# Performance work log

Hardware: AMD Instinct MI355X
Metric: run time of the kernel (lower is better)

The kernel has to match this reference:

```python
import jax, jax.numpy as jnp
import numpy as np

B, F_IN, GRID, D, C = 32768, 64, 8, 16, 10
N = GRID * GRID          # 64 nodes
HID = N * D              # 1024
ATOMS = 2
LN_EPS = 1e-5
EPS = 1e-8


def _layernorm(h):
    mu = h.mean(-1, keepdims=True)
    var = h.var(-1, keepdims=True)
    return (h - mu) / jnp.sqrt(var + LN_EPS)


def _regulator(sig, w1, b1, g, be, w2, b2):
    # Linear -> LayerNorm -> Tanh -> Linear -> Sigmoid
    h = jnp.tanh(_layernorm(sig @ w1.T + b1) * g + be)
    return jax.nn.sigmoid(h @ w2.T + b2)


def _reg_params(key, in_dim):
    k = jax.random.split(key, 4)
    return (jax.random.normal(k[0], (16, in_dim)) * 0.3,
            jax.random.normal(k[1], (16,)) * 0.1,
            jnp.ones((16,)), jnp.zeros((16,)),
            jax.random.normal(k[2], (3, 16)) * 0.3,
            jax.random.normal(k[3], (3,)) * 0.1)


def setup_inputs() -> dict:
    key = jax.random.key(0)
    ks = jax.random.split(key, 16)
    # 2D grid 4-neighbour adjacency mask (constant)
    mask = np.zeros((N, N), np.float32)
    for i in range(N):
        r, c = divmod(i, GRID)
        if r > 0: mask[i, i - GRID] = 1
        if r < GRID - 1: mask[i, i + GRID] = 1
        if c > 0: mask[i, i - 1] = 1
        if c < GRID - 1: mask[i, i + 1] = 1
    pr = _reg_params(ks[10], 3)
    cr = _reg_params(ks[11], 3)
    sr = _reg_params(ks[12], 3)
    scr = _reg_params(ks[13], 2)
    inp = {
        "x": jax.random.normal(ks[0], (B, F_IN)),
        "W_embed": jax.random.normal(ks[1], (HID, F_IN)) * 0.1,
        "b_embed": jnp.zeros((HID,)),
        "adj_weights": jax.random.normal(ks[2], (N, N)) * 0.1,
        "adj_mask": jnp.asarray(mask),
        "V_slow": jax.random.normal(ks[3], (D, D)) * 0.1,
        "W_slow": jax.random.normal(ks[4], (D, D)) * 0.1,
        "gate_w": jax.random.normal(ks[5], (1, D)) * 0.3,
        "gate_b": jnp.zeros((1,)),
        "W_fast": jax.random.normal(ks[6], (D, D)) * 0.05,  # buffer, eval mode (no Hebbian update)
        "basis": jax.random.normal(ks[7], (ATOMS, D)) * 0.5,
        "Wq": jax.random.normal(ks[8], (D, D)) * 0.2,
        "sc_w1": jax.random.normal(ks[9], (8, HID)) * 0.05,
        "sc_w2": jax.random.normal(ks[14], (4, 8)) * 0.3,
        "W_read": jax.random.normal(ks[15], (C, HID)) * 0.05,
        "b_read": jnp.zeros((C,)),
    }
    for pre, p in (("pr", pr), ("cr", cr), ("sr", sr), ("scr", scr)):
        for nm, v in zip(("w1", "b1", "g", "be", "w2", "b2"), p):
            inp[pre + "_" + nm] = v
    return inp


def reference(x, W_embed, b_embed, adj_weights, adj_mask,
              pr_w1, pr_b1, pr_g, pr_be, pr_w2, pr_b2,
              V_slow, W_slow, gate_w, gate_b, W_fast,
              cr_w1, cr_b1, cr_g, cr_be, cr_w2, cr_b2,
              basis, Wq,
              sr_w1, sr_b1, sr_g, sr_be, sr_w2, sr_b2,
              sc_w1, sc_w2,
              scr_w1, scr_b1, scr_g, scr_be, scr_w2, scr_b2,
              W_read, b_read):
    Bx = x.shape[0]
    x_embed = (x @ W_embed.T + b_embed).reshape(Bx, N, D)

    # --- AutoregulatedPlasticity adjacency ---
    sig = jnp.stack([jnp.var(x, ddof=1), jnp.abs(x_embed).mean(),
                     jnp.linalg.norm(adj_weights)])[None]
    pl = _regulator(sig, pr_w1, pr_b1, pr_g, pr_be, pr_w2, pr_b2)[0]
    adj = jax.nn.sigmoid(adj_weights * pl[0]) * adj_mask
    adj = adj / jnp.clip(adj.sum(1, keepdims=True), 1e-6, None)
    x_agg = jnp.einsum('nm,bmd->bnd', adj, x_embed)

    # --- AutoregulatedContinuum (eval: W_fast fixed) ---
    xf = x_agg.reshape(-1, D)           # [B*N, D]
    v = xf @ V_slow.T
    sig = jnp.stack([jnp.var(xf, ddof=1), jnp.abs(v).mean(),
                     jnp.linalg.norm(W_slow)])[None]
    ctrl = _regulator(sig, cr_w1, cr_b1, cr_g, cr_be, cr_w2, cr_b2)[0]
    gate = jax.nn.sigmoid(v @ gate_w.T + gate_b) * ctrl[0]   # [B*N, 1]
    fast_out = xf @ W_fast.T
    x_proc = (gate * (v + fast_out * ctrl[2])).reshape(Bx, N, D)

    # --- AutoregulatedSymbiotic, applied per node (vmapped over node axis) ---
    ortho = jnp.linalg.norm(basis @ basis.T - jnp.eye(ATOMS))
    scale = D ** 0.5 + EPS

    def sym_one(xn):  # xn: [B, D]
        w = jax.nn.softmax((xn @ Wq.T) @ basis.T / scale, axis=-1)  # [B, ATOMS]
        ent = -(w * jnp.log(w + EPS)).sum(-1).mean()
        sig_n = jnp.stack([jnp.var(xn, ddof=1), ent, ortho])[None]
        infl = _regulator(sig_n, sr_w1, sr_b1, sr_g, sr_be, sr_w2, sr_b2)[0, 0]
        return (1.0 - infl) * xn + infl * (w @ basis), ent

    refined, ents = jax.vmap(sym_one)(x_proc.transpose(1, 0, 2))  # [N,B,D]
    x_proc = refined.transpose(1, 0, 2)
    entropy = ents[-1]  # torch loop keeps the last node's entropy

    x_flat = x_proc.reshape(Bx, HID)
    logits = x_flat @ W_read.T + b_read

    # --- AutoregulatedSupConHead (entropy.item() -> detached scalar) ---
    sigc = jnp.stack([jnp.var(x_flat, ddof=1),
                      jax.lax.stop_gradient(entropy)])[None]
    gain = _regulator(sigc, scr_w1, scr_b1, scr_g, scr_be, scr_w2, scr_b2)[0, 0]
    proj = (jax.nn.relu(x_flat @ sc_w1.T) @ sc_w2.T) * gain
    return logits, proj, entropy, ortho
```

## Files before the change

kernel.cpp:

```cpp
#include <hip/hip_runtime.h>

typedef unsigned short u16;
typedef __attribute__((ext_vector_type(8))) short short8;
typedef __attribute__((ext_vector_type(4))) float f32x4;

#define MFMA16(a,b,c) __builtin_amdgcn_mfma_f32_16x16x32_bf16(a,b,c,0,0,0)

#define B_SZ   32768
#define NNODE  64
#define NB_PAIR (B_SZ*NNODE)
#define OUT_PROJ   327680
#define OUT_ENT    458752
#define OUT_ORTHO  458753

#define OFF_SCAL   ((size_t)0)
#define OFF_ADJ    ((size_t)512)
#define OFF_BEFF   (OFF_ADJ  + 8192u)
#define OFF_WEFF   (OFF_BEFF + 4096u)
#define OFF_WCAT   (OFF_WEFF + 131072u)
#define OFF_S1     (OFF_WCAT + 65536u)
#define OFF_S2     (OFF_S1   + 12288u)
#define OFF_S3     (OFF_S2   + 12288u)
#define OFF_S4     (OFF_S3   + 2048u*192u*4u)
#define OFF_H      (OFF_S4   + 8192u)
#define OFF_W01    (OFF_H    + (size_t)B_SZ*8u*4u)
#define OFF_CAN    (OFF_W01  + (size_t)NB_PAIR*4u)

#define CAN_X      0u
#define CAN_WEMB   2097152u
#define CAN_WREAD  (CAN_WEMB + 65536u)
#define CAN_SCW1   (CAN_WREAD + 10240u)
#define CAN_SMALL  (CAN_SCW1 + 8192u)
#define CAN_TOTAL  (CAN_SMALL + 11008u)
#define OFF_BEX    (((OFF_CAN + (size_t)CAN_TOTAL*2u) + 63u) & ~(size_t)63u)
#define OFF_WET    (OFF_BEX + 48u*16u*2u)
#define OFF_VW     (OFF_WET + 131072u)
#define OFF_VB     (OFF_VW  + 131072u)
#define OFF_WC     (OFF_VB  + 4096u)
#define OFF_SW     (OFF_WC  + 131072u)
#define OFF_BC2    (OFF_SW  + 24576u)
#define OFF_SB     (OFF_BC2 + 4096u)
#define OFF_DR     (OFF_SB  + 1024u)
#define WS_NEEDED  (OFF_DR  + 192u*8u)

__device__ __forceinline__ float bf2f(u16 u){
    unsigned v = ((unsigned)u) << 16;
    return __builtin_bit_cast(float, v);
}
__device__ __forceinline__ u16 f2bf(float f){
    unsigned u = __builtin_bit_cast(unsigned, f);
    u += 0x7FFFu + ((u >> 16) & 1u);
    return (u16)(u >> 16);
}
__device__ __forceinline__ float sigm(float x){ return 1.f/(1.f + expf(-x)); }
__device__ __forceinline__ u16 conv_one(const void* src, int i, int isfp32){
    return isfp32 ? f2bf(((const float*)src)[i]) : ((const u16*)src)[i];
}
__device__ __forceinline__ void store_out(void* dout, int idx, float v, int isfp32){
    if (isfp32) ((float*)dout)[idx] = v;
    else        ((u16*)dout)[idx]   = f2bf(v);
}
__device__ __forceinline__ double blk_red(double v, double* sred, int tid){
    #pragma unroll
    for (int off = 32; off > 0; off >>= 1) v += __shfl_xor(v, off);
    if ((tid & 63) == 0) sred[tid >> 6] = v;
    __syncthreads();
    double r = sred[0] + sred[1] + sred[2] + sred[3];
    __syncthreads();
    return r;
}

__device__ void run_regulator(const u16* w1, const u16* b1, const u16* g,
                              const u16* be, const u16* w2, const u16* b2,
                              const float* sig, int in_dim, float* out)
{
    float h[16];
    float mu = 0.f;
    for (int i = 0; i < 16; ++i){
        float a = bf2f(b1[i]);
        for (int j = 0; j < in_dim; ++j) a += sig[j]*bf2f(w1[i*in_dim + j]);
        h[i] = a; mu += a;
    }
    mu *= 0.0625f;
    float var = 0.f;
    for (int i = 0; i < 16; ++i){ float d = h[i]-mu; var += d*d; }
    var *= 0.0625f;
    float inv = 1.f / sqrtf(var + 1e-5f);
    for (int i = 0; i < 16; ++i){
        float hn = (h[i]-mu)*inv;
        h[i] = tanhf(hn*bf2f(g[i]) + bf2f(be[i]));
    }
    for (int c = 0; c < 3; ++c){
        float o = bf2f(b2[c]);
        for (int i = 0; i < 16; ++i) o += h[i]*bf2f(w2[c*16 + i]);
        out[c] = sigm(o);
    }
}

__device__ __forceinline__ int probe_isfp32(const u16* xraw, int tid, int* sred)
{
    int c = 0;
    #pragma unroll
    for (int j = 0; j < 4; ++j){
        u16 u = xraw[(tid*4 + j)*2];
        int e = (u >> 7) & 0xFF;
        if (u == 0 || (e >= 90 && e <= 140)) c++;
    }
    #pragma unroll
    for (int off = 32; off > 0; off >>= 1) c += __shfl_xor(c, off);
    if ((tid & 63) == 0) sred[tid >> 6] = c;
    __syncthreads();
    int tot = sred[0]+sred[1]+sred[2]+sred[3];
    __syncthreads();
    return tot < 614;
}

__global__ __launch_bounds__(256) void kc_big(const void* x, const void* wemb,
    const void* wread, const void* scw1, u16* can, float* scal)
{
    __shared__ int sred[4];
    int tid = threadIdx.x;
    int isfp32 = probe_isfp32((const u16*)x, tid, sred);
    if (blockIdx.x == 0 && tid == 0) scal[127] = isfp32 ? 1.0f : 0.0f;
    int gid = blockIdx.x*256 + tid, stride = gridDim.x*256;
    for (int i = gid; i < 2097152; i += stride) can[CAN_X + i]     = conv_one(x, i, isfp32);
    for (int i = gid; i < 65536;   i += stride) can[CAN_WEMB + i]  = conv_one(wemb, i, isfp32);
    for (int i = gid; i < 10240;   i += stride) can[CAN_WREAD + i] = conv_one(wread, i, isfp32);
    for (int i = gid; i < 8192;    i += stride) can[CAN_SCW1 + i]  = conv_one(scw1, i, isfp32);
}

struct SmallTab { const void* src[36]; int cnt[36]; int off[36]; };
__global__ __launch_bounds__(256) void kc_small(SmallTab t, u16* can, const float* scal)
{
    int isfp32 = scal[127] != 0.f;
    int gid = blockIdx.x*256 + threadIdx.x, stride = gridDim.x*256;
    for (int e = 0; e < 36; ++e){
        const void* s = t.src[e];
        u16* d = can + t.off[e];
        int n = t.cnt[e];
        for (int i = gid; i < n; i += stride) d[i] = conv_one(s, i, isfp32);
    }
}

__global__ __launch_bounds__(256) void k0_wcat(const u16* wread, const u16* scw1,
    const u16* wemb, const u16* vslow, const u16* gatew, u16* wcat, u16* wembT, u16* bex)
{
    int b = blockIdx.x, tid = threadIdx.x;
    if (b < 128){
        int idx = b*256 + tid;
        int row = idx >> 10, k = idx & 1023;
        u16 v = 0;
        if (row < 10)      v = wread[row*1024 + k];
        else if (row < 18) v = scw1[(row-10)*1024 + k];
        wcat[idx] = v;
    } else if (b < 384){
        int idx = (b-128)*256 + tid;
        int m = idx >> 10, jj = idx & 1023;
        wembT[jj*64 + m] = wemb[m*1024 + jj];
    } else {
        if (tid < 16){
            float a = 0.f;
            for (int i = 0; i < 16; ++i) a += bf2f(gatew[i])*bf2f(vslow[i*16+tid]);
            bex[32*16+tid] = f2bf(a);
        }
    }
}

__global__ __launch_bounds__(256) void k1_embed(const u16* x, const u16* wemb,
                                                const u16* bemb, float* s1)
{
    __shared__ float red[12];
    int tid = threadIdx.x, wave = tid>>6, lane = tid&63;
    int m = lane&15, quad = lane>>4;
    int cg = blockIdx.x & 31, rc = blockIdx.x >> 5;
    int col0 = cg*32 + m, col1 = col0 + 16;
    short8 b00 = *(const short8*)(wemb + col0*64 + quad*8);
    short8 b01 = *(const short8*)(wemb + col0*64 + quad*8 + 32);
    short8 b10 = *(const short8*)(wemb + col1*64 + quad*8);
    short8 b11 = *(const short8*)(wemb + col1*64 + quad*8 + 32);
    float bias0 = bf2f(bemb[col0]), bias1 = bf2f(bemb[col1]);
    float sx = 0.f, sxx = 0.f, sabs = 0.f;
    const u16* xbase = x + (size_t)(rc*1024 + wave*256 + m)*64 + quad*8;
    #pragma unroll 4
    for (int it = 0; it < 16; ++it){
        const u16* xr = xbase + (size_t)it*16*64;
        short8 a0 = *(const short8*)xr;
        short8 a1 = *(const short8*)(xr + 32);
        if (cg == 0){
            #pragma unroll
            for (int j = 0; j < 8; ++j){
                float f0 = bf2f((u16)a0[j]); sx += f0; sxx += f0*f0;
                float f1 = bf2f((u16)a1[j]); sx += f1; sxx += f1*f1;
            }
        }
        f32x4 zc = {0.f,0.f,0.f,0.f};
        f32x4 c0 = MFMA16(a0, b00, zc);
        c0 = MFMA16(a1, b01, c0);
        f32x4 c1 = MFMA16(a0, b10, zc);
        c1 = MFMA16(a1, b11, c1);
        #pragma unroll
        for (int r = 0; r < 4; ++r)
            sabs += fabsf(c0[r]+bias0) + fabsf(c1[r]+bias1);
    }
    #pragma unroll
    for (int off = 32; off > 0; off >>= 1){
        sx   += __shfl_xor(sx, off);
        sxx  += __shfl_xor(sxx, off);
        sabs += __shfl_xor(sabs, off);
    }
    if (lane == 0){ red[wave*3] = sx; red[wave*3+1] = sxx; red[wave*3+2] = sabs; }
    __syncthreads();
    if (tid == 0){
        for (int k = 0; k < 3; ++k)
            s1[blockIdx.x*3 + k] = red[k] + red[3+k] + red[6+k] + red[9+k];
    }
}

__global__ __launch_bounds__(256) void k2_adj(const u16* adjw, const u16* adjm, const u16* bemb,
    const u16* w1, const u16* b1, const u16* g, const u16* be, const u16* w2, const u16* b2,
    const float* s1, float* scal, u16* adjb, float* beff)
{
    __shared__ double sred[4];
    __shared__ float raw[4096];
    __shared__ float rowsum[64];
    __shared__ float bembs[1024];
    __shared__ float pl0s;
    int tid = threadIdx.x;
    for (int i = tid; i < 1024; i += 256) bembs[i] = bf2f(bemb[i]);
    double s=0, ss=0, sa=0;
    for (int i = tid; i < 1024; i += 256){
        s += (double)s1[i*3]; ss += (double)s1[i*3+1]; sa += (double)s1[i*3+2];
    }
    double nq = 0;
    for (int i = tid; i < 4096; i += 256){ float f = bf2f(adjw[i]); nq += (double)(f*f); }
    double S  = blk_red(s,  sred, tid);
    double SS = blk_red(ss, sred, tid);
    double SA = blk_red(sa, sred, tid);
    double NQ = blk_red(nq, sred, tid);
    if (tid == 0){
        double nx = 2097152.0;
        float sg[3];
        sg[0] = (float)((SS - S*S/nx)/(nx - 1.0));
        sg[1] = (float)(SA / 33554432.0);
        sg[2] = sqrtf((float)NQ);
        float o[3];
        run_regulator(w1,b1,g,be,w2,b2, sg, 3, o);
        scal[0] = o[0]; pl0s = o[0];
    }
    __syncthreads();
    float pl0 = pl0s;
    for (int i = tid; i < 4096; i += 256)
        raw[i] = sigm(bf2f(adjw[i])*pl0) * bf2f(adjm[i]);
    __syncthreads();
    if (tid < 64){
        float r = 0.f;
        for (int mc = 0; mc < 64; ++mc) r += raw[tid*64 + mc];
        rowsum[tid] = fmaxf(r, 1e-6f);
    }
    __syncthreads();
    for (int i = tid; i < 4096; i += 256) adjb[i] = f2bf(raw[i] / rowsum[i>>6]);
    for (int o = tid; o < 1024; o += 256){
        int n = o >> 4, d = o & 15;
        float a = 0.f;
        for (int m = 0; m < 64; ++m) a += raw[n*64+m]*bembs[m*16+d];
        beff[o] = a / rowsum[n];
    }
}

__global__ __launch_bounds__(256) void k2b_mfma(const u16* adjb, const u16* wembT, u16* weff)
{
    int tid = threadIdx.x, wave = tid>>6, lane = tid&63;
    int m = lane&15, quad = lane>>4;
    const u16* ar = adjb + (wave*16 + m)*64 + quad*8;
    short8 a0 = *(const short8*)ar;
    short8 a1 = *(const short8*)(ar + 32);
    int col = blockIdx.x*16 + m;
    const u16* br = wembT + col*64 + quad*8;
    short8 b0 = *(const short8*)br;
    short8 b1 = *(const short8*)(br + 32);
    f32x4 acc = {0.f,0.f,0.f,0.f};
    acc = MFMA16(a0, b0, acc);
    acc = MFMA16(a1, b1, acc);
    #pragma unroll
    for (int r = 0; r < 4; ++r)
        weff[(size_t)(wave*16 + quad*4 + r)*1024 + blockIdx.x*16 + m] = f2bf(acc[r]);
}

__global__ __launch_bounds__(256) void kvw(const u16* vslow, const u16* weff, const float* beff,
                                           u16* vw, float* vbias)
{
    __shared__ float Vs[256];
    int tid = threadIdx.x, b = blockIdx.x;
    Vs[tid] = bf2f(vslow[tid]);
    __syncthreads();
    if (b < 256){
        int idx = b*256 + tid;
        int j = idx >> 6, kf = idx & 63;
        int n = j >> 4, i = j & 15;
        float a = 0.f;
        #pragma unroll
        for (int d = 0; d < 16; ++d) a += Vs[i*16+d]*bf2f(weff[(size_t)(n*16+d)*64 + kf]);
        vw[(size_t)j*64 + kf] = f2bf(a);
    } else {
        int o = (b-256)*256 + tid;
        int n = o >> 4, i = o & 15;
        float a = 0.f;
        #pragma unroll
        for (int d = 0; d < 16; ++d) a += Vs[i*16+d]*beff[n*16+d];
        vbias[o] = a;
    }
}

__global__ __launch_bounds__(256) void k3_stats(const u16* x, const u16* weff, const float* beff,
                                                const u16* vw, const float* vbias, float* s2)
{
    __shared__ float red[12];
    int tid = threadIdx.x, wave = tid>>6, lane = tid&63;
    int m = lane&15, quad = lane>>4;
    int cg = blockIdx.x & 31, rc = blockIdx.x >> 5;
    int col0 = cg*32 + m, col1 = col0 + 16;
    short8 b00 = *(const short8*)(weff + (size_t)col0*64 + quad*8);
    short8 b01 = *(const short8*)(weff + (size_t)col0*64 + quad*8 + 32);
    short8 b10 = *(const short8*)(weff + (size_t)col1*64 + quad*8);
    short8 b11 = *(const short8*)(weff + (size_t)col1*64 + quad*8 + 32);
    short8 v00 = *(const short8*)(vw + (size_t)col0*64 + quad*8);
    short8 v01 = *(const short8*)(vw + (size_t)col0*64 + quad*8 + 32);
    short8 v10 = *(const short8*)(vw + (size_t)col1*64 + quad*8);
    short8 v11 = *(const short8*)(vw + (size_t)col1*64 + quad*8 + 32);
    float be0 = beff[col0], be1 = beff[col1];
    float vb0 = vbias[col0], vb1 = vbias[col1];
    float psum=0.f, pssq=0.f, pabsv=0.f;
    const u16* xbase = x + (size_t)(rc*1024 + wave*256 + m)*64 + quad*8;
    #pragma unroll 4
    for (int it = 0; it < 16; ++it){
        const u16* xr = xbase + (size_t)it*16*64;
        short8 a0 = *(const short8*)xr;
        short8 a1 = *(const short8*)(xr + 32);
        f32x4 zc = {0.f,0.f,0.f,0.f};
        f32x4 c0 = MFMA16(a0, b00, zc);
        c0 = MFMA16(a1, b01, c0);
        f32x4 c1 = MFMA16(a0, b10, zc);
        c1 = MFMA16(a1, b11, c1);
        f32x4 w0 = MFMA16(a0, v00, zc);
        w0 = MFMA16(a1, v01, w0);
        f32x4 w1 = MFMA16(a0, v10, zc);
        w1 = MFMA16(a1, v11, w1);
        #pragma unroll
        for (int r = 0; r < 4; ++r){
            float f0 = c0[r] + be0, f1 = c1[r] + be1;
            psum += f0 + f1; pssq += f0*f0 + f1*f1;
            pabsv += fabsf(w0[r] + vb0) + fabsf(w1[r] + vb1);
        }
    }
    #pragma unroll
    for (int off = 32; off > 0; off >>= 1){
        psum  += __shfl_xor(psum, off);
        pssq  += __shfl_xor(pssq, off);
        pabsv += __shfl_xor(pabsv, off);
    }
    if (lane == 0){ red[wave*3] = psum; red[wave*3+1] = pssq; red[wave*3+2] = pabsv; }
    __syncthreads();
    if (tid == 0){
        for (int k = 0; k < 3; ++k)
            s2[blockIdx.x*3 + k] = red[k] + red[3+k] + red[6+k] + red[9+k];
    }
}

__global__ __launch_bounds__(256) void k3b_ctrl(const u16* wslow,
    const u16* vslow, const u16* wfast, const u16* wq, const u16* basis,
    const u16* w1, const u16* b1, const u16* g, const u16* be, const u16* w2, const u16* b2,
    const float* s2, float* scal, u16* bex)
{
    __shared__ double sred[4];
    __shared__ float ctrl2s;
    int tid = threadIdx.x;
    double s=0, ss=0, sv=0;
    for (int i = tid; i < 1024; i += 256){
        s += (double)s2[i*3]; ss += (double)s2[i*3+1]; sv += (double)s2[i*3+2];
    }
    float wf = bf2f(wslow[tid]);
    double nq = (double)(wf*wf);
    double S  = blk_red(s,  sred, tid);
    double SS = blk_red(ss, sred, tid);
    double SV = blk_red(sv, sred, tid);
    double NQ = blk_red(nq, sred, tid);
    if (tid == 0){
        double M = 33554432.0;
        float sg[3];
        sg[0] = (float)((SS - S*S/M)/(M - 1.0));
        sg[1] = (float)(SV / M);
        sg[2] = sqrtf((float)NQ);
        float o[3];
        run_regulator(w1,b1,g,be,w2,b2, sg, 3, o);
        scal[1] = o[0]; scal[2] = o[2];
        ctrl2s = o[2];
    }
    __syncthreads();
    float ctrl2 = ctrl2s;
    if (tid < 64){
        #pragma unroll
        for (int j = 0; j < 4; ++j){
            int idx = tid*4 + j;
            int d = idx >> 4, k = idx & 15;
            bex[(16+d)*16+k] = f2bf(bf2f(vslow[idx]) + ctrl2*bf2f(wfast[idx]));
        }
    } else if (tid < 96){
        int a = (tid-64) >> 4, k = (tid-64) & 15;
        float e = 0.f;
        for (int d = 0; d < 16; ++d){
            float bq = 0.f;
            for (int j = 0; j < 16; ++j) bq += bf2f(basis[a*16+j])*bf2f(wq[j*16+d]);
            e += bq*(bf2f(vslow[d*16+k]) + ctrl2*bf2f(wfast[d*16+k]));
        }
        bex[(33+a)*16+k] = f2bf(0.25f*e);
    }
}

__global__ __launch_bounds__(256) void kbw(const u16* bex, const u16* weff, const float* beff,
                                           const u16* gateb, u16* wc, u16* sw,
                                           float* bc, float* sb)
{
    __shared__ float BcL[256], gvL[16], e0L[16], e1L[16];
    int tid = threadIdx.x;
    if (tid < 256) BcL[tid] = bf2f(bex[(16 + (tid>>4))*16 + (tid&15)]);
    if (tid < 16){
        gvL[tid] = bf2f(bex[32*16+tid]);
        e0L[tid] = bf2f(bex[33*16+tid]);
        e1L[tid] = bf2f(bex[34*16+tid]);
    }
    __syncthreads();
    int id = blockIdx.x*256 + tid;
    if (id < 65536){
        int col = id >> 6, k = id & 63;
        int n = col >> 4, d = col & 15;
        float a = 0.f;
        #pragma unroll
        for (int dd = 0; dd < 16; ++dd)
            a += BcL[d*16+dd]*bf2f(weff[(size_t)(n*16+dd)*64 + k]);
        wc[(size_t)col*64 + k] = f2bf(a);
    } else if (id < 77824){
        int j2 = id - 65536;
        int scol = j2 >> 6, k = j2 & 63;
        int n = scol/3, j = scol - n*3;
        const float* sr = (j==0) ? gvL : (j==1) ? e0L : e1L;
        float a = 0.f;
        #pragma unroll
        for (int dd = 0; dd < 16; ++dd)
            a += sr[dd]*bf2f(weff[(size_t)(n*16+dd)*64 + k]);
        sw[(size_t)scol*64 + k] = f2bf(a);
    } else if (id < 78848){
        int col = id - 77824;
        int n = col >> 4, d = col & 15;
        float a = 0.f;
        #pragma unroll
        for (int dd = 0; dd < 16; ++dd) a += BcL[d*16+dd]*beff[n*16+dd];
        bc[col] = a;
    } else if (id < 79040){
        int s = id - 78848;
        int n = s/3, j = s - n*3;
        const float* sr = (j==0) ? gvL : (j==1) ? e0L : e1L;
        float a = 0.f;
        #pragma unroll
        for (int dd = 0; dd < 16; ++dd) a += sr[dd]*beff[n*16+dd];
        if (j == 0) a += bf2f(gateb[0]);
        sb[s] = a;
    }
}

#define SCP 193
__global__ __launch_bounds__(256) void k4_stats(const u16* x, const u16* wc, const u16* sw,
    const float* bc, const float* sb, const float* scal, unsigned* wpack, float* s3)
{
    __shared__ float sc[16*SCP];
    __shared__ float gt[1024];
    __shared__ float entp[256];
    __shared__ float snode[128];
    int tid = threadIdx.x, wave = tid>>6, lane = tid&63;
    int m = lane&15, quad = lane>>4;
    int row0 = blockIdx.x*16;
    const u16* xr = x + (row0 + m)*64 + quad*8;
    short8 a0 = *(const short8*)xr;
    short8 a1 = *(const short8*)(xr + 32);
    float ctrl0 = scal[1];
    #pragma unroll
    for (int tt = 0; tt < 3; ++tt){
        int ct = wave*3 + tt;
        int scol = ct*16 + m;
        const u16* br = sw + (size_t)scol*64 + quad*8;
        short8 b0 = *(const short8*)br;
        short8 b1 = *(const short8*)(br + 32);
        f32x4 zc = {0.f,0.f,0.f,0.f};
        f32x4 c = MFMA16(a0, b0, zc);
        c = MFMA16(a1, b1, c);
        float sbv = sb[scol];
        #pragma unroll
        for (int r = 0; r < 4; ++r)
            sc[(quad*4+r)*SCP + scol] = c[r] + sbv;
    }
    __syncthreads();
    {
        int n = tid & 63, rgrp = tid >> 6;
        float ent = 0.f;
        #pragma unroll
        for (int rr = 0; rr < 4; ++rr){
            int row = rgrp*4 + rr;
            float gd  = sc[row*SCP + 3*n];
            float e0d = sc[row*SCP + 3*n + 1];
            float e1d = sc[row*SCP + 3*n + 2];
            float gate = ctrl0 / (1.f + __expf(-gd));
            float l0 = gate*e0d, l1 = gate*e1d;
            float w1v = 1.f/(1.f + __expf(l0 - l1));
            float w0v = 1.f - w1v;
            ent += -(w0v*__logf(w0v + 1e-8f) + w1v*__logf(w1v + 1e-8f));
            gt[row*64 + n] = gate;
            wpack[(size_t)(row0 + row)*64 + n] =
                ((unsigned)f2bf(w0v) << 16) | (unsigned)f2bf(gate);
        }
        entp[tid] = ent;
    }
    __syncthreads();
    #pragma unroll
    for (int tt = 0; tt < 16; ++tt){
        int n = wave*16 + tt;
        int col = n*16 + m;
        const u16* br = wc + (size_t)col*64 + quad*8;
        short8 b0 = *(const short8*)br;
        short8 b1 = *(const short8*)(br + 32);
        f32x4 zc = {0.f,0.f,0.f,0.f};
        f32x4 c = MFMA16(a0, b0, zc);
        c = MFMA16(a1, b1, c);
        float bcv = bc[col];
        float ps = 0.f, pq = 0.f;
        #pragma unroll
        for (int r = 0; r < 4; ++r){
            float gate = gt[(quad*4+r)*64 + n];
            float xp = gate*(c[r] + bcv);
            ps += xp; pq += xp*xp;
        }
        #pragma unroll
        for (int off = 32; off > 0; off >>= 1){
            ps += __shfl_xor(ps, off);
            pq += __shfl_xor(pq, off);
        }
        if (lane == 0){ snode[n] = ps; snode[64+n] = pq; }
    }
    __syncthreads();
    if (tid < 192){
        float v;
        if (tid < 128) v = snode[tid];
        else { int n = tid-128; v = entp[n]+entp[64+n]+entp[128+n]+entp[192+n]; }
        s3[(size_t)blockIdx.x*192 + tid] = v;
    }
}

__global__ __launch_bounds__(256) void k5a_red(const float* s3, double* dred)
{
    __shared__ double sred[4];
    int tid = threadIdx.x, col = blockIdx.x;
    double a = 0;
    for (int i = tid; i < 2048; i += 256) a += (double)s3[(size_t)i*192 + col];
    #pragma unroll
    for (int off = 32; off > 0; off >>= 1) a += __shfl_xor(a, off);
    if ((tid & 63) == 0) sred[tid >> 6] = a;
    __syncthreads();
    if (tid == 0) dred[col] = sred[0]+sred[1]+sred[2]+sred[3];
}

__global__ __launch_bounds__(64) void k5b_infl(const u16* basis,
    const u16* w1, const u16* b1, const u16* g, const u16* be, const u16* w2, const u16* b2,
    const double* dred, float* scal, void* dout)
{
    int n = threadIdx.x;
    int isfp32 = scal[127] != 0.f;
    double sum = dred[n], ssq = dred[64+n], ent = dred[128+n];
    double Mn = 524288.0;
    float varn = (float)((ssq - sum*sum/Mn)/(Mn - 1.0));
    float entm = (float)(ent / 32768.0);
    float b0[16], b1v[16];
    for (int d = 0; d < 16; ++d){ b0[d] = bf2f(basis[d]); b1v[d] = bf2f(basis[16+d]); }
    float g00=0.f, g01=0.f, g11=0.f;
    for (int d = 0; d < 16; ++d){ g00 += b0[d]*b0[d]; g01 += b0[d]*b1v[d]; g11 += b1v[d]*b1v[d]; }
    float ortho = sqrtf((g00-1.f)*(g00-1.f) + 2.f*g01*g01 + (g11-1.f)*(g11-1.f));
    float sg[3] = {varn, entm, ortho};
    float o[3];
    run_regulator(w1,b1,g,be,w2,b2, sg, 3, o);
    scal[4+n] = o[0];
    if (n == 63){ scal[68] = entm;  store_out(dout, OUT_ENT,   entm,  isfp32); }
    if (n == 0) { scal[69] = ortho; store_out(dout, OUT_ORTHO, ortho, isfp32); }
}

#define XSP 132
__global__ __launch_bounds__(256) void k6_read(const u16* x, const unsigned* wpack,
    const u16* wc, const float* bc, const u16* wcat,
    const u16* basis, const u16* bread, const float* scal,
    void* dout, float* hbuf, float* s4)
{
    __shared__ unsigned gwP[32*65];
    __shared__ u16 xs[4*16*XSP];
    __shared__ float comb[2*64*9];
    __shared__ float infl_s[64], b0s[16], b1s[16], brd[16];
    __shared__ float red[8];
    int tid = threadIdx.x;
    int isfp32 = scal[127] != 0.f;
    for (int i = tid; i < 2048; i += 256)
        gwP[(i >> 6)*65 + (i & 63)] = wpack[(size_t)blockIdx.x*2048 + i];
    if (tid < 64) infl_s[tid] = scal[4+tid];
    if (tid < 16){
        b0s[tid] = bf2f(basis[tid]);
        b1s[tid] = bf2f(basis[16+tid]);
        brd[tid] = (tid < 10) ? bf2f(bread[tid]) : 0.f;
    }
    __syncthreads();
    int wave = tid>>6, lane = tid&63;
    int m = lane&15, quad = lane>>4;
    int rowgrp = wave & 1, half = wave >> 1;
    int row = blockIdx.x*32 + rowgrp*16 + m;
    const u16* xr = x + (size_t)row*64 + quad*8;
    short8 a0 = *(const short8*)xr;
    short8 a1 = *(const short8*)(xr + 32);
    u16* xsw = xs + wave*16*XSP;
    f32x4 acc0 = {0.f,0.f,0.f,0.f}, acc1 = {0.f,0.f,0.f,0.f};
    float psum = 0.f, pssq = 0.f;
    for (int cc = 0; cc < 4; ++cc){
        int c8 = half*4 + cc;
        #pragma unroll
        for (int t = 0; t < 8; ++t){
            int n = c8*8 + t;
            int col = n*16 + m;
            const u16* br = wc + (size_t)col*64 + quad*8;
            short8 b0 = *(const short8*)br;
            short8 b1 = *(const short8*)(br + 32);
            f32x4 zc = {0.f,0.f,0.f,0.f};
            f32x4 c = MFMA16(a0, b0, zc);
            c = MFMA16(a1, b1, c);
            float bcv = bc[col];
            float fi = infl_s[n], om = 1.f - fi;
            #pragma unroll
            for (int r = 0; r < 4; ++r){
                unsigned gv = gwP[(rowgrp*16 + quad*4 + r)*65 + n];
                float gate = bf2f((u16)(gv & 0xFFFFu));
                float w0v  = bf2f((u16)(gv >> 16));
                float xp = gate*(c[r] + bcv);
                float xf = om*xp + fi*(w0v*b0s[m] + (1.f-w0v)*b1s[m]);
                psum += xf; pssq += xf*xf;
                xsw[(quad*4+r)*XSP + t*16 + m] = f2bf(xf);
            }
        }
        #pragma unroll
        for (int kk = 0; kk < 4; ++kk){
            short8 af = *(const short8*)(xsw + m*XSP + kk*32 + quad*8);
            short8 bb0 = *(const short8*)(wcat + m*1024      + c8*128 + kk*32 + quad*8);
            short8 bb1 = *(const short8*)(wcat + (16+m)*1024 + c8*128 + kk*32 + quad*8);
            acc0 = MFMA16(af, bb0, acc0);
            acc1 = MFMA16(af, bb1, acc1);
        }
    }
    if (half){
        float* cb = comb + (rowgrp*64 + lane)*9;
        #pragma unroll
        for (int r = 0; r < 4; ++r){ cb[r] = acc0[r]; cb[4+r] = acc1[r]; }
    }
    __syncthreads();
    if (!half){
        const float* cb = comb + (rowgrp*64 + lane)*9;
        int rowbase = blockIdx.x*32 + rowgrp*16 + quad*4;
        #pragma unroll
        for (int r = 0; r < 4; ++r){
            float o0 = acc0[r] + cb[r];
            float o1 = acc1[r] + cb[4+r];
            int rowg = rowbase + r;
            if (m < 10) store_out(dout, rowg*10 + m, o0 + brd[m], isfp32);
            else        hbuf[rowg*8 + (m-10)] = fmaxf(o0, 0.f);
            if (m < 2)  hbuf[rowg*8 + 6 + m]  = fmaxf(o1, 0.f);
        }
    }
    #pragma unroll
    for (int off = 32; off > 0; off >>= 1){
        psum += __shfl_xor(psum, off);
        pssq += __shfl_xor(pssq, off);
    }
    if (lane == 0){ red[wave] = psum; red[4+wave] = pssq; }
    __syncthreads();
    if (tid == 0){
        s4[blockIdx.x*2]   = red[0]+red[1]+red[2]+red[3];
        s4[blockIdx.x*2+1] = red[4]+red[5]+red[6]+red[7];
    }
}

__global__ __launch_bounds__(256) void k8_proj(const float* hbuf, const u16* scw2,
    const u16* w1, const u16* b1, const u16* g, const u16* be, const u16* w2, const u16* b2,
    const float* s4, const float* scal, void* dout)
{
    __shared__ double sred[4];
    __shared__ float w2s[32];
    __shared__ float gains;
    int tid = threadIdx.x;
    int isfp32 = scal[127] != 0.f;
    if (tid < 32) w2s[tid] = bf2f(scw2[tid]);
    double s=0, ss=0;
    for (int i = tid; i < 1024; i += 256){ s += (double)s4[i*2]; ss += (double)s4[i*2+1]; }
    double S  = blk_red(s,  sred, tid);
    double SS = blk_red(ss, sred, tid);
    if (tid == 0){
        double M = 33554432.0;
        float sg[2];
        sg[0] = (float)((SS - S*S/M)/(M - 1.0));
        sg[1] = scal[68];
        float o[3];
        run_regulator(w1,b1,g,be,w2,b2, sg, 2, o);
        gains = o[0];
    }
    __syncthreads();
    float gain = gains;
    int b = blockIdx.x*256 + tid;
    const float* h = hbuf + (size_t)b*8;
    float hv[8];
    #pragma unroll
    for (int k = 0; k < 8; ++k) hv[k] = h[k];
    #pragma unroll
    for (int i = 0; i < 4; ++i){
        float o = 0.f;
        #pragma unroll
        for (int k = 0; k < 8; ++k) o += hv[k]*w2s[i*8+k];
        store_out(dout, OUT_PROJ + b*4 + i, o*gain, isfp32);
    }
}

extern "C" void kernel_launch(void* const* d_in, const int* in_sizes, int n_in,
                              void* d_out, int out_size, void* d_ws, size_t ws_size,
                              hipStream_t stream)
{
    if (ws_size < WS_NEEDED) return;

    char* ws = (char*)d_ws;
    float* scal  = (float*)(ws + OFF_SCAL);
    u16*   adjb  = (u16*)  (ws + OFF_ADJ);
    float* beff  = (float*)(ws + OFF_BEFF);
    u16*   weff  = (u16*)  (ws + OFF_WEFF);
    u16*   wcat  = (u16*)  (ws + OFF_WCAT);
    float* s1    = (float*)(ws + OFF_S1);
    float* s2    = (float*)(ws + OFF_S2);
    float* s3    = (float*)(ws + OFF_S3);
    float* s4    = (float*)(ws + OFF_S4);
    float* hbuf  = (float*)(ws + OFF_H);
    unsigned* wpack = (unsigned*)(ws + OFF_W01);
    u16*   can   = (u16*)  (ws + OFF_CAN);
    u16*   bex   = (u16*)  (ws + OFF_BEX);
    u16*   wembT = (u16*)  (ws + OFF_WET);
    u16*   vw    = (u16*)  (ws + OFF_VW);
    float* vbias = (float*)(ws + OFF_VB);
    u16*   wc    = (u16*)  (ws + OFF_WC);
    u16*   sw    = (u16*)  (ws + OFF_SW);
    float* bc    = (float*)(ws + OFF_BC2);
    float* sb    = (float*)(ws + OFF_SB);
    double* dred = (double*)(ws + OFF_DR);

    static const int sidx[36] = {2,3,4,5,6,7,8,9,10,11,13,15,
        16,17,18,19,20,21, 22,23,24,25,26,27, 28,29,30,31,32,33, 34,35,36,37,38,39};
    static const int scnt[36] = {1024,4096,4096,256,256,16,1,256,32,256,32,10,
        48,16,16,16,48,3, 48,16,16,16,48,3, 48,16,16,16,48,3, 32,16,16,16,48,3};
    SmallTab t;
    const u16* canp[40];
    {
        int off = (int)CAN_SMALL;
        for (int j = 0; j < 36; ++j){
            t.src[j] = d_in[sidx[j]];
            t.cnt[j] = scnt[j];
            t.off[j] = off;
            canp[sidx[j]] = can + off;
            off += (scnt[j] + 7) & ~7;
        }
    }
    canp[0]  = can + CAN_X;
    canp[1]  = can + CAN_WEMB;
    canp[12] = can + CAN_SCW1;
    canp[14] = can + CAN_WREAD;

    const u16* pr_[6]; const u16* cr_[6]; const u16* sr_[6]; const u16* sc_[6];
    for (int i = 0; i < 6; ++i){
        pr_[i] = canp[16+i]; cr_[i] = canp[22+i];
        sr_[i] = canp[28+i]; sc_[i] = canp[34+i];
    }

    kc_big  <<<1024,256, 0, stream>>>(d_in[0], d_in[1], d_in[14], d_in[12], can, scal);
    kc_small<<<16,  256, 0, stream>>>(t, can, scal);
    k0_wcat <<<385, 256, 0, stream>>>(canp[14], canp[12], canp[1], canp[5], canp[7],
                 wcat, wembT, bex);
    k1_embed<<<1024,256, 0, stream>>>(canp[0], canp[1], canp[2], s1);
    k2_adj  <<<1,   256, 0, stream>>>(canp[3], canp[4], canp[2],
                 pr_[0],pr_[1],pr_[2],pr_[3],pr_[4],pr_[5], s1, scal, adjb, beff);
    k2b_mfma<<<64,  256, 0, stream>>>(adjb, wembT, weff);
    kvw     <<<260, 256, 0, stream>>>(canp[5], weff, beff, vw, vbias);
    k3_stats<<<1024,256, 0, stream>>>(canp[0], weff, beff, vw, vbias, s2);
    k3b_ctrl<<<1,   256, 0, stream>>>(canp[6], canp[5], canp[9], canp[11], canp[10],
                 cr_[0],cr_[1],cr_[2],cr_[3],cr_[4],cr_[5], s2, scal, bex);
    kbw     <<<312, 256, 0, stream>>>(bex, weff, beff, canp[8], wc, sw, bc, sb);
    k4_stats<<<2048,256, 0, stream>>>(canp[0], wc, sw, bc, sb, scal, wpack, s3);
    k5a_red <<<192, 256, 0, stream>>>(s3, dred);
    k5b_infl<<<1,   64,  0, stream>>>(canp[10],
                 sr_[0],sr_[1],sr_[2],sr_[3],sr_[4],sr_[5], dred, scal, d_out);
    k6_read <<<1024,256, 0, stream>>>(canp[0], wpack, wc, bc, wcat, canp[10], canp[15],
                 scal, d_out, hbuf, s4);
    k8_proj <<<128, 256, 0, stream>>>(hbuf, canp[13],
                 sc_[0],sc_[1],sc_[2],sc_[3],sc_[4],sc_[5], s4, scal, d_out);
}
```

Baseline: 352.2 us.

## Give each wave all 64 nodes in k6_read, halving blocks and dropping cross-wave combine

k6_read now processes 64 rows per block, with each wave owning 16 rows across all 8 node chunks. Previously two waves split the node range per row group and merged partial sums through shared memory plus a barrier. The MFMA operands are swapped so each lane holds 4 consecutive d-values, which lets the bf16 results be packed into one 64-bit LDS store, and the bias comes in as a vector load. The trade-off is that each wave has a longer serial loop, more registers are live, and the grid is half as large (512 blocks), which may reduce parallelism.

```diff
diff --git a/kernel.cpp b/kernel.cpp
--- a/kernel.cpp
+++ b/kernel.cpp
@@ -1,6 +1,7 @@
 #include <hip/hip_runtime.h>
 
 typedef unsigned short u16;
+typedef unsigned long long u64;
 typedef __attribute__((ext_vector_type(8))) short short8;
 typedef __attribute__((ext_vector_type(4))) float f32x4;
 
@@ -589,21 +590,20 @@
     if (n == 0) { scal[69] = ortho; store_out(dout, OUT_ORTHO, ortho, isfp32); }
 }
 
-#define XSP 132
-__global__ __launch_bounds__(256) void k6_read(const u16* x, const unsigned* wpack,
+#define XSP 136
+__global__ __launch_bounds__(256, 2) void k6_read(const u16* x, const unsigned* wpack,
     const u16* wc, const float* bc, const u16* wcat,
     const u16* basis, const u16* bread, const float* scal,
     void* dout, float* hbuf, float* s4)
 {
-    __shared__ unsigned gwP[32*65];
-    __shared__ u16 xs[4*16*XSP];
-    __shared__ float comb[2*64*9];
+    __shared__ unsigned gwP[64*65];
+    __shared__ __align__(16) u16 xs[4*16*XSP];
     __shared__ float infl_s[64], b0s[16], b1s[16], brd[16];
     __shared__ float red[8];
     int tid = threadIdx.x;
     int isfp32 = scal[127] != 0.f;
-    for (int i = tid; i < 2048; i += 256)
-        gwP[(i >> 6)*65 + (i & 63)] = wpack[(size_t)blockIdx.x*2048 + i];
+    for (int i = tid; i < 4096; i += 256)
+        gwP[(i >> 6)*65 + (i & 63)] = wpack[(size_t)blockIdx.x*4096 + i];
     if (tid < 64) infl_s[tid] = scal[4+tid];
     if (tid < 16){
         b0s[tid] = bf2f(basis[tid]);
@@ -613,38 +613,51 @@
     __syncthreads();
     int wave = tid>>6, lane = tid&63;
     int m = lane&15, quad = lane>>4;
-    int rowgrp = wave & 1, half = wave >> 1;
-    int row = blockIdx.x*32 + rowgrp*16 + m;
+    int row = blockIdx.x*64 + wave*16 + m;
     const u16* xr = x + (size_t)row*64 + quad*8;
     short8 a0 = *(const short8*)xr;
     short8 a1 = *(const short8*)(xr + 32);
+    float b0d[4], b1d[4];
+    #pragma unroll
+    for (int r = 0; r < 4; ++r){ b0d[r] = b0s[quad*4+r]; b1d[r] = b1s[quad*4+r]; }
     u16* xsw = xs + wave*16*XSP;
+    const unsigned* gwrow = gwP + (wave*16 + m)*65;
     f32x4 acc0 = {0.f,0.f,0.f,0.f}, acc1 = {0.f,0.f,0.f,0.f};
     float psum = 0.f, pssq = 0.f;
-    for (int cc = 0; cc < 4; ++cc){
-        int c8 = half*4 + cc;
+    for (int c8 = 0; c8 < 8; ++c8){
+        f32x4 cT[8], bc4[8];
+        unsigned gv[8];
+        float fiv[8];
         #pragma unroll
         for (int t = 0; t < 8; ++t){
             int n = c8*8 + t;
             int col = n*16 + m;
             const u16* br = wc + (size_t)col*64 + quad*8;
-            short8 b0 = *(const short8*)br;
-            short8 b1 = *(const short8*)(br + 32);
+            short8 wf0 = *(const short8*)br;
+            short8 wf1 = *(const short8*)(br + 32);
             f32x4 zc = {0.f,0.f,0.f,0.f};
-            f32x4 c = MFMA16(a0, b0, zc);
-            c = MFMA16(a1, b1, c);
-            float bcv = bc[col];
-            float fi = infl_s[n], om = 1.f - fi;
+            f32x4 cc = MFMA16(wf0, a0, zc);
+            cc = MFMA16(wf1, a1, cc);
+            cT[t] = cc;
+            bc4[t] = *(const f32x4*)(bc + n*16 + quad*4);
+            gv[t]  = gwrow[n];
+            fiv[t] = infl_s[n];
+        }
+        #pragma unroll
+        for (int t = 0; t < 8; ++t){
+            float gate = bf2f((u16)(gv[t] & 0xFFFFu));
+            float w0v  = bf2f((u16)(gv[t] >> 16));
+            float fi = fiv[t], om = 1.f - fi;
+            u64 pk = 0;
             #pragma unroll
             for (int r = 0; r < 4; ++r){
-                unsigned gv = gwP[(rowgrp*16 + quad*4 + r)*65 + n];
-                float gate = bf2f((u16)(gv & 0xFFFFu));
-                float w0v  = bf2f((u16)(gv >> 16));
-                float xp = gate*(c[r] + bcv);
-                float xf = om*xp + fi*(w0v*b0s[m] + (1.f-w0v)*b1s[m]);
+                float xp = gate*(cT[t][r] + bc4[t][r]);
+                float bb = w0v*b0d[r] + (1.f - w0v)*b1d[r];
+                float xf = om*xp + fi*bb;
                 psum += xf; pssq += xf*xf;
-                xsw[(quad*4+r)*XSP + t*16 + m] = f2bf(xf);
+                pk |= ((u64)f2bf(xf)) << (r*16);
             }
+            *(u64*)(xsw + m*XSP + t*16 + quad*4) = pk;
         }
         #pragma unroll
         for (int kk = 0; kk < 4; ++kk){
@@ -655,24 +668,13 @@
             acc1 = MFMA16(af, bb1, acc1);
         }
     }
-    if (half){
-        float* cb = comb + (rowgrp*64 + lane)*9;
-        #pragma unroll
-        for (int r = 0; r < 4; ++r){ cb[r] = acc0[r]; cb[4+r] = acc1[r]; }
-    }
-    __syncthreads();
-    if (!half){
-        const float* cb = comb + (rowgrp*64 + lane)*9;
-        int rowbase = blockIdx.x*32 + rowgrp*16 + quad*4;
-        #pragma unroll
-        for (int r = 0; r < 4; ++r){
-            float o0 = acc0[r] + cb[r];
-            float o1 = acc1[r] + cb[4+r];
-            int rowg = rowbase + r;
-            if (m < 10) store_out(dout, rowg*10 + m, o0 + brd[m], isfp32);
-            else        hbuf[rowg*8 + (m-10)] = fmaxf(o0, 0.f);
-            if (m < 2)  hbuf[rowg*8 + 6 + m]  = fmaxf(o1, 0.f);
-        }
+    int rowbase = blockIdx.x*64 + wave*16 + quad*4;
+    #pragma unroll
+    for (int r = 0; r < 4; ++r){
+        int rowg = rowbase + r;
+        if (m < 10) store_out(dout, rowg*10 + m, acc0[r] + brd[m], isfp32);
+        else        hbuf[rowg*8 + (m-10)] = fmaxf(acc0[r], 0.f);
+        if (m < 2)  hbuf[rowg*8 + 6 + m]  = fmaxf(acc1[r], 0.f);
     }
     #pragma unroll
     for (int off = 32; off > 0; off >>= 1){
@@ -698,7 +700,7 @@
     int isfp32 = scal[127] != 0.f;
     if (tid < 32) w2s[tid] = bf2f(scw2[tid]);
     double s=0, ss=0;
-    for (int i = tid; i < 1024; i += 256){ s += (double)s4[i*2]; ss += (double)s4[i*2+1]; }
+    for (int i = tid; i < 512; i += 256){ s += (double)s4[i*2]; ss += (double)s4[i*2+1]; }
     double S  = blk_red(s,  sred, tid);
     double SS = blk_red(ss, sred, tid);
     if (tid == 0){
@@ -799,7 +801,7 @@
     k5a_red <<<192, 256, 0, stream>>>(s3, dred);
     k5b_infl<<<1,   64,  0, stream>>>(canp[10],
                  sr_[0],sr_[1],sr_[2],sr_[3],sr_[4],sr_[5], dred, scal, d_out);
-    k6_read <<<1024,256, 0, stream>>>(canp[0], wpack, wc, bc, wcat, canp[10], canp[15],
+    k6_read <<<512, 256, 0, stream>>>(canp[0], wpack, wc, bc, wcat, canp[10], canp[15],
                  scal, d_out, hbuf, s4);
     k8_proj <<<128, 256, 0, stream>>>(hbuf, canp[13],
                  sc_[0],sc_[1],sc_[2],sc_[3],sc_[4],sc_[5], s4, scal, d_out);
```

Result: no change. 346.0 us (-1.7%).
